# Optimization experiments

Measured on AMD Instinct MI355X. Metric: run time of the kernel, lower is better.

The kernel has to match this reference:

```python
import jax, jax.numpy as jnp
import numpy as np

N_NODES = 50000
N_EDGES = 800000
IN_C = 16
HID_C = 16
OUT_C = 10
N_GRAPHS = 500
EDGE_DIM = 3
MLP_HID = 25
BN_EPS = 1e-5


def setup_inputs() -> dict:
    key = jax.random.key(0)
    ks = iter(jax.random.split(key, 40))

    def nrm(shape, scale=1.0):
        return jax.random.normal(next(ks), shape, dtype=jnp.float32) * scale

    inp = {}
    inp["x"] = nrm((N_NODES, IN_C))
    inp["edge_index"] = jax.random.randint(next(ks), (2, N_EDGES), 0, N_NODES, dtype=jnp.int32)
    inp["edge_attr"] = jax.random.uniform(next(ks), (N_EDGES, EDGE_DIM), dtype=jnp.float32)
    inp["batch"] = jnp.sort(jax.random.randint(next(ks), (N_NODES,), 0, N_GRAPHS, dtype=jnp.int32))

    def bn_params():
        g = jax.random.uniform(next(ks), (MLP_HID,), minval=0.8, maxval=1.2, dtype=jnp.float32)
        b = nrm((MLP_HID,), 0.1)
        mu = nrm((MLP_HID,), 0.1)
        var = jax.random.uniform(next(ks), (MLP_HID,), minval=0.5, maxval=1.5, dtype=jnp.float32)
        return g, b, mu, var

    # edge MLP 1: 3 -> 25 -> IN_C*HID_C
    inp["W1a"] = nrm((EDGE_DIM, MLP_HID), 0.3)
    inp["b1a"] = nrm((MLP_HID,), 0.05)
    inp["g1"], inp["bt1"], inp["m1"], inp["v1"] = bn_params()
    inp["W1b"] = nrm((MLP_HID, IN_C * HID_C), 0.1)
    inp["b1b"] = nrm((IN_C * HID_C,), 0.05)
    inp["root1"] = nrm((IN_C, HID_C), 0.2)
    inp["bias1"] = nrm((HID_C,), 0.05)

    # edge MLP 2: 3 -> 25 -> HID_C*HID_C
    inp["W2a"] = nrm((EDGE_DIM, MLP_HID), 0.3)
    inp["b2a"] = nrm((MLP_HID,), 0.05)
    inp["g2"], inp["bt2"], inp["m2"], inp["v2"] = bn_params()
    inp["W2b"] = nrm((MLP_HID, HID_C * HID_C), 0.1)
    inp["b2b"] = nrm((HID_C * HID_C,), 0.05)
    inp["root2"] = nrm((HID_C, HID_C), 0.2)
    inp["bias2"] = nrm((HID_C,), 0.05)

    # final MLP([HID_C, OUT_C]) -> single plain linear (plain_last)
    inp["fcW"] = nrm((HID_C, OUT_C), 0.2)
    inp["fcb"] = nrm((OUT_C,), 0.05)
    return inp


def _edge_mlp(e, Wa, ba, g, bt, mu, var, Wb, bb):
    # Linear -> BatchNorm(eval) -> ReLU -> (dropout=eval identity) -> Linear
    h = e @ Wa + ba
    h = g * (h - mu) * jax.lax.rsqrt(var + BN_EPS) + bt
    h = jax.nn.relu(h)
    return h @ Wb + bb


def _nnconv(x, src, dst, w_edge, root, bias, out_dim):
    # message: x_j [E,in] times per-edge weight [E,in,out]
    msg = jnp.einsum("ei,eio->eo", x[src], w_edge)
    agg = jax.ops.segment_sum(msg, dst, num_segments=N_NODES)
    deg = jax.ops.segment_sum(jnp.ones((src.shape[0],), msg.dtype), dst, num_segments=N_NODES)
    agg = agg / jnp.maximum(deg, 1.0)[:, None]  # mean aggregation
    return agg + x @ root + bias


def reference(x, edge_index, edge_attr, batch,
              W1a, b1a, g1, bt1, m1, v1, W1b, b1b, root1, bias1,
              W2a, b2a, g2, bt2, m2, v2, W2b, b2b, root2, bias2,
              fcW, fcb):
    src, dst = edge_index[0], edge_index[1]

    w1 = _edge_mlp(edge_attr, W1a, b1a, g1, bt1, m1, v1, W1b, b1b).reshape(-1, IN_C, HID_C)
    x = jax.nn.elu(_nnconv(x, src, dst, w1, root1, bias1, HID_C))

    w2 = _edge_mlp(edge_attr, W2a, b2a, g2, bt2, m2, v2, W2b, b2b).reshape(-1, HID_C, HID_C)
    x = jax.nn.elu(_nnconv(x, src, dst, w2, root2, bias2, HID_C))

    # global mean pooling over graphs
    pooled = jax.ops.segment_sum(x, batch, num_segments=N_GRAPHS)
    cnt = jax.ops.segment_sum(jnp.ones((x.shape[0],), x.dtype), batch, num_segments=N_GRAPHS)
    pooled = pooled / jnp.maximum(cnt, 1.0)[:, None]

    return pooled @ fcW + fcb  # [N_GRAPHS, OUT_C]
```

## Files before the change

### kernel.cpp

```cpp
#include <hip/hip_runtime.h>
#include <math.h>

#define N_NODES 50000
#define N_EDGES 800000
#define IN_C 16
#define HID_C 16
#define OUT_C 10
#define N_GRAPHS 500
#define EDGE_DIM 3
#define MLP_HID 25
#define BN_EPS 1e-5f

#define SCAN_NB ((N_NODES + 255) / 256)

typedef __attribute__((ext_vector_type(8))) short short8;
typedef __attribute__((ext_vector_type(4))) float f32x4;
union U4S8 { uint4 u; short8 s; };


__global__ __launch_bounds__(256) void prep_graph_kernel(
    const float* __restrict__ W1a, const float* __restrict__ b1a,
    const float* __restrict__ g1, const float* __restrict__ bt1,
    const float* __restrict__ m1, const float* __restrict__ v1,
    const float* __restrict__ W2a, const float* __restrict__ b2a,
    const float* __restrict__ g2, const float* __restrict__ bt2,
    const float* __restrict__ m2, const float* __restrict__ v2,
    const int* __restrict__ batch,
    float* __restrict__ AC1, float* __restrict__ AC2,
    int* __restrict__ goff)
{
    int t = threadIdx.x;
    if (blockIdx.x == 0) {
        if (t < 26) {
            int k = t;
            if (k < 25) {
                float sc = g1[k] / sqrtf(v1[k] + BN_EPS);
                AC1[k*4+0] = sc * W1a[0*MLP_HID+k];
                AC1[k*4+1] = sc * W1a[1*MLP_HID+k];
                AC1[k*4+2] = sc * W1a[2*MLP_HID+k];
                AC1[k*4+3] = sc * (b1a[k] - m1[k]) + bt1[k];
            } else {
                AC1[100] = 0.f; AC1[101] = 0.f; AC1[102] = 0.f; AC1[103] = 1.f;
            }
        } else if (t >= 32 && t < 58) {
            int k = t - 32;
            if (k < 25) {
                float sc = g2[k] / sqrtf(v2[k] + BN_EPS);
                AC2[k*4+0] = sc * W2a[0*MLP_HID+k];
                AC2[k*4+1] = sc * W2a[1*MLP_HID+k];
                AC2[k*4+2] = sc * W2a[2*MLP_HID+k];
                AC2[k*4+3] = sc * (b2a[k] - m2[k]) + bt2[k];
            } else {
                AC2[100] = 0.f; AC2[101] = 0.f; AC2[102] = 0.f; AC2[103] = 1.f;
            }
        }
    }
    int g = blockIdx.x * blockDim.x + t;
    if (g <= N_GRAPHS) {
        int lo = 0, hi = N_NODES;
        while (lo < hi) {
            int mid = (lo + hi) >> 1;
            if (batch[mid] < g) lo = mid + 1; else hi = mid;
        }
        goff[g] = lo;
    }
}

__global__ __launch_bounds__(256) void pack_w_kernel(
    const float* __restrict__ W1b, const float* __restrict__ b1b,
    const float* __restrict__ W2b, const float* __restrict__ b2b,
    unsigned int* __restrict__ WHI1, unsigned int* __restrict__ WLO1,
    unsigned int* __restrict__ WHI2, unsigned int* __restrict__ WLO2)
{
    int t = blockIdx.x * 256 + threadIdx.x;
    if (t >= 1664) return;
    const float *Wb, *bb; unsigned int *WH, *WL;
    int tl = t;
    if (t < 832) { Wb = W1b; bb = b1b; WH = WHI1; WL = WLO1; }
    else { tl = t - 832; Wb = W2b; bb = b2b; WH = WHI2; WL = WLO2; }
    int m = tl >> 6;
    int L = tl & 63;
    int q = L >> 4, o = L & 15;
    unsigned int hi[8], lo[8];
    for (int j = 0; j < 8; ++j) {
        int kp = m*32 + q*8 + j;
        int k = kp >> 4, i = kp & 15;
        float w = (k < 25) ? Wb[k*256 + i*16 + o] : bb[i*16 + o];
        unsigned int u = __float_as_uint(w);
        unsigned int h = (u + 0x7FFFu + ((u >> 16) & 1u)) >> 16;
        hi[j] = h;
        float rl = w - __uint_as_float(h << 16);
        unsigned int ul = __float_as_uint(rl);
        lo[j] = (ul + 0x7FFFu + ((ul >> 16) & 1u)) >> 16;
    }
    int base = (m*64 + L) * 4;
    for (int d = 0; d < 4; ++d) {
        WH[base + d] = hi[2*d] | (hi[2*d+1] << 16);
        WL[base + d] = lo[2*d] | (lo[2*d+1] << 16);
    }
}


__global__ __launch_bounds__(256) void rank_kernel(const int* __restrict__ dst,
                                                   int* __restrict__ cnt,
                                                   int* __restrict__ rank) {
    int e = blockIdx.x * blockDim.x + threadIdx.x;
    if (e < N_EDGES) rank[e] = atomicAdd(&cnt[dst[e]], 1);
}

__global__ __launch_bounds__(256) void scan_p1(const int* __restrict__ cnt,
                                               int* __restrict__ bsum) {
    __shared__ int lds[256];
    int t = threadIdx.x;
    int idx = blockIdx.x * 256 + t;
    lds[t] = (idx < N_NODES) ? cnt[idx] : 0;
    __syncthreads();
    for (int d = 128; d > 0; d >>= 1) {
        if (t < d) lds[t] += lds[t + d];
        __syncthreads();
    }
    if (t == 0) bsum[blockIdx.x] = lds[0];
}

__global__ __launch_bounds__(256) void scan_p2(const int* __restrict__ bsum,
                                               int* __restrict__ bpre,
                                               int* __restrict__ off) {
    __shared__ int lds[256];
    int t = threadIdx.x;
    lds[t] = (t < SCAN_NB) ? bsum[t] : 0;
    __syncthreads();
    for (int d = 1; d < 256; d <<= 1) {
        int v = (t >= d) ? lds[t - d] : 0;
        __syncthreads();
        lds[t] += v;
        __syncthreads();
    }
    if (t < SCAN_NB) bpre[t] = (t > 0) ? lds[t - 1] : 0;
    if (t == 255) off[N_NODES] = lds[255];
}

__global__ __launch_bounds__(256) void scan_p3(const int* __restrict__ cnt,
                                               const int* __restrict__ bpre,
                                               int* __restrict__ off) {
    __shared__ int lds[256];
    int t = threadIdx.x;
    int idx = blockIdx.x * 256 + t;
    int v = (idx < N_NODES) ? cnt[idx] : 0;
    lds[t] = v;
    __syncthreads();
    for (int d = 1; d < 256; d <<= 1) {
        int u = (t >= d) ? lds[t - d] : 0;
        __syncthreads();
        lds[t] += u;
        __syncthreads();
    }
    if (idx < N_NODES) off[idx] = bpre[blockIdx.x] + lds[t] - v;
}


__global__ __launch_bounds__(256) void edge_mfma_kernel(
    const float* __restrict__ xin,
    const int* __restrict__ src, const int* __restrict__ dst,
    const int* __restrict__ rank, const int* __restrict__ off,
    const float* __restrict__ eattr,
    const float* __restrict__ AC,
    const unsigned int* __restrict__ WHI, const unsigned int* __restrict__ WLO,
    float* __restrict__ msg_buf)
{
    __shared__ uint4 wlo_s[832];
    __shared__ float ac_s[104];
    __shared__ __attribute__((aligned(16))) float xs_s[4][16][16];
    __shared__ __attribute__((aligned(16))) float ea_s[4][16][4];
    __shared__ int   pp_s[4][16];

    const int tid = threadIdx.x;
    #pragma unroll
    for (int it = 0; it < 4; ++it) {
        int gi = tid + it*256;
        if (gi < 832) wlo_s[gi] = ((const uint4*)WLO)[gi];
    }
    if (tid < 104) ac_s[tid] = AC[tid];
    __syncthreads();

    const int wave = tid >> 6;
    const int lane = tid & 63;
    const int q = lane >> 4;

    short8 whi[13];
    #pragma unroll
    for (int m = 0; m < 13; ++m) {
        U4S8 c; c.u = ((const uint4*)WHI)[m*64 + lane];
        whi[m] = c.s;
    }

    const int tile = blockIdx.x * 4 + wave;
    const int e0 = tile * 16;

    {
        int el = lane >> 2, part = lane & 3;
        int s = src[e0 + el];
        const float4 v = ((const float4*)(xin + (size_t)s * IN_C))[part];
        *(float4*)&xs_s[wave][el][part*4] = v;
    }
    if (lane < 48) {
        int c = lane >> 4, e = lane & 15;
        ea_s[wave][e][c] = eattr[(size_t)(e0 + e)*3 + c];
    }
    if (lane < 16) {
        int e = e0 + lane;
        pp_s[wave][lane] = off[dst[e]] + rank[e];
    }

    const int e = lane & 15;
    const int i0 = (q & 1) * 8;
    const float4 ea = *(const float4*)&ea_s[wave][e][0];
    const float a0 = ea.x, a1 = ea.y, a2 = ea.z;
    float x8[8];
    {
        float4 v0 = *(const float4*)&xs_s[wave][e][i0];
        float4 v1 = *(const float4*)&xs_s[wave][e][i0 + 4];
        x8[0]=v0.x; x8[1]=v0.y; x8[2]=v0.z; x8[3]=v0.w;
        x8[4]=v1.x; x8[5]=v1.y; x8[6]=v1.z; x8[7]=v1.w;
    }

    f32x4 acc = {0.f, 0.f, 0.f, 0.f};
    #pragma unroll
    for (int m = 0; m < 13; ++m) {
        int k = 2*m + (q >> 1);
        const float4 A = *(const float4*)&ac_s[k*4];
        float hk = fmaxf(fmaf(a2, A.z, fmaf(a1, A.y, fmaf(a0, A.x, A.w))), 0.f);
        unsigned int pd0, pd1, pd2, pd3;
        {
            unsigned int b0 = __float_as_uint(hk * x8[0]);
            unsigned int b1 = __float_as_uint(hk * x8[1]);
            pd0 = __builtin_amdgcn_perm(b1, b0, 0x07060302u);
            unsigned int b2 = __float_as_uint(hk * x8[2]);
            unsigned int b3 = __float_as_uint(hk * x8[3]);
            pd1 = __builtin_amdgcn_perm(b3, b2, 0x07060302u);
            unsigned int b4 = __float_as_uint(hk * x8[4]);
            unsigned int b5 = __float_as_uint(hk * x8[5]);
            pd2 = __builtin_amdgcn_perm(b5, b4, 0x07060302u);
            unsigned int b6 = __float_as_uint(hk * x8[6]);
            unsigned int b7 = __float_as_uint(hk * x8[7]);
            pd3 = __builtin_amdgcn_perm(b7, b6, 0x07060302u);
        }
        U4S8 af; af.u = make_uint4(pd0, pd1, pd2, pd3);
        U4S8 wl; wl.u = wlo_s[m*64 + lane];
        acc = __builtin_amdgcn_mfma_f32_16x16x32_bf16(af.s, whi[m], acc, 0, 0, 0);
        acc = __builtin_amdgcn_mfma_f32_16x16x32_bf16(af.s, wl.s,   acc, 0, 0, 0);
    }

    const int o = lane & 15;
    #pragma unroll
    for (int r = 0; r < 4; ++r) {
        int p = pp_s[wave][q*4 + r];
        msg_buf[(size_t)p * HID_C + o] = acc[r];
    }
}

__global__ __launch_bounds__(256) void node_gather_kernel(
    const float* __restrict__ xin, const float* __restrict__ msg_buf,
    const int* __restrict__ off,
    const float* __restrict__ root, const float* __restrict__ bias,
    float* __restrict__ xout)
{
    int t = blockIdx.x * blockDim.x + threadIdx.x;
    int n = t >> 4;
    int o = t & 15;
    if (n >= N_NODES) return;
    int lo = off[n], hi = off[n+1];
    float inv = 1.f / fmaxf((float)(hi - lo), 1.f);

    float s0 = 0.f, s1 = 0.f, s2 = 0.f, s3 = 0.f;
    int r = lo;
    for (; r + 4 <= hi; r += 4) {
        s0 += msg_buf[(size_t)r     * HID_C + o];
        s1 += msg_buf[(size_t)(r+1) * HID_C + o];
        s2 += msg_buf[(size_t)(r+2) * HID_C + o];
        s3 += msg_buf[(size_t)(r+3) * HID_C + o];
    }
    for (; r < hi; ++r) s0 += msg_buf[(size_t)r * HID_C + o];
    float s = (s0 + s1) + (s2 + s3);

    float acc = fmaf(s, inv, bias[o]);
    const float* xr = xin + (size_t)n * IN_C;
    #pragma unroll
    for (int i = 0; i < IN_C; ++i)
        acc = fmaf(xr[i], root[i*HID_C+o], acc);
    xout[(size_t)n*HID_C + o] = acc > 0.f ? acc : (expf(acc) - 1.f);
}

__global__ __launch_bounds__(64) void pool_final_kernel(
    const float* __restrict__ xin, const int* __restrict__ goff,
    const float* __restrict__ fcW, const float* __restrict__ fcb,
    float* __restrict__ out)
{
    __shared__ float part[4][HID_C];
    __shared__ float pooled[HID_C];
    int g = blockIdx.x;
    int t = threadIdx.x;
    int c = t & 15, sub = t >> 4;
    int lo = goff[g], hi = goff[g+1];
    float s = 0.f;
    for (int n = lo + sub; n < hi; n += 4)
        s += xin[(size_t)n*HID_C + c];
    part[sub][c] = s;
    __syncthreads();
    if (t < HID_C) {
        pooled[t] = (part[0][t] + part[1][t] + part[2][t] + part[3][t])
                    / fmaxf((float)(hi - lo), 1.f);
    }
    __syncthreads();
    if (t < OUT_C) {
        float acc = fcb[t];
        #pragma unroll
        for (int i = 0; i < HID_C; ++i)
            acc = fmaf(pooled[i], fcW[i*OUT_C+t], acc);
        out[g*OUT_C + t] = acc;
    }
}


extern "C" void kernel_launch(void* const* d_in, const int* in_sizes, int n_in,
                              void* d_out, int out_size, void* d_ws, size_t ws_size,
                              hipStream_t stream)
{
    const float* x     = (const float*)d_in[0];
    const int*   ei    = (const int*)d_in[1];
    const float* eattr = (const float*)d_in[2];
    const int*   batch = (const int*)d_in[3];
    const float* W1a   = (const float*)d_in[4];
    const float* b1a   = (const float*)d_in[5];
    const float* g1    = (const float*)d_in[6];
    const float* bt1   = (const float*)d_in[7];
    const float* m1    = (const float*)d_in[8];
    const float* v1    = (const float*)d_in[9];
    const float* W1b   = (const float*)d_in[10];
    const float* b1b   = (const float*)d_in[11];
    const float* root1 = (const float*)d_in[12];
    const float* bias1 = (const float*)d_in[13];
    const float* W2a   = (const float*)d_in[14];
    const float* b2a   = (const float*)d_in[15];
    const float* g2    = (const float*)d_in[16];
    const float* bt2   = (const float*)d_in[17];
    const float* m2    = (const float*)d_in[18];
    const float* v2    = (const float*)d_in[19];
    const float* W2b   = (const float*)d_in[20];
    const float* b2b   = (const float*)d_in[21];
    const float* root2 = (const float*)d_in[22];
    const float* bias2 = (const float*)d_in[23];
    const float* fcW   = (const float*)d_in[24];
    const float* fcb   = (const float*)d_in[25];

    const int* src = ei;
    const int* dst = ei + N_EDGES;

    float* ws   = (float*)d_ws;
    float* MSG  = ws;
    float* X1   = ws + 12800000;
    float* X2   = ws + 13600000;
    int*   RANK = (int*)(ws + 14400000);
    int*   CNT  = (int*)(ws + 15200000);
    int*   OFF  = (int*)(ws + 15250000);
    int*   GOFF = (int*)(ws + 15300064);
    unsigned int* WHI1 = (unsigned int*)(ws + 15300576);
    unsigned int* WLO1 = (unsigned int*)(ws + 15303904);
    unsigned int* WHI2 = (unsigned int*)(ws + 15307232);
    unsigned int* WLO2 = (unsigned int*)(ws + 15310560);
    float* AC1  = ws + 15313888;
    float* AC2  = ws + 15314000;
    int*   BSUM = (int*)(ws + 15314112);
    int*   BPRE = (int*)(ws + 15314368);

    hipMemsetAsync(CNT, 0, N_NODES * sizeof(int), stream);
    prep_graph_kernel<<<3, 256, 0, stream>>>(W1a, b1a, g1, bt1, m1, v1,
                                             W2a, b2a, g2, bt2, m2, v2,
                                             batch, AC1, AC2, GOFF);
    pack_w_kernel<<<7, 256, 0, stream>>>(W1b, b1b, W2b, b2b,
                                         WHI1, WLO1, WHI2, WLO2);
    rank_kernel<<<N_EDGES/256, 256, 0, stream>>>(dst, CNT, RANK);
    scan_p1<<<SCAN_NB, 256, 0, stream>>>(CNT, BSUM);
    scan_p2<<<1, 256, 0, stream>>>(BSUM, BPRE, OFF);
    scan_p3<<<SCAN_NB, 256, 0, stream>>>(CNT, BPRE, OFF);

    edge_mfma_kernel<<<N_EDGES/64, 256, 0, stream>>>(x, src, dst, RANK, OFF,
                                                     eattr, AC1, WHI1, WLO1, MSG);
    node_gather_kernel<<<(N_NODES*16+255)/256, 256, 0, stream>>>(x, MSG, OFF,
                                                                 root1, bias1, X1);

    edge_mfma_kernel<<<N_EDGES/64, 256, 0, stream>>>(X1, src, dst, RANK, OFF,
                                                     eattr, AC2, WHI2, WLO2, MSG);
    node_gather_kernel<<<(N_NODES*16+255)/256, 256, 0, stream>>>(X1, MSG, OFF,
                                                                 root2, bias2, X2);

    pool_final_kernel<<<N_GRAPHS, 64, 0, stream>>>(X2, GOFF, fcW, fcb, (float*)d_out);
}
```

Before: 309.9 us.

## Precompute edge scatter positions and process four edge tiles per wave

A new small kernel computes each edge's final scatter position (off[dst]+rank) once and stores it, so both edge passes read it directly instead of recomputing it through a dependent gather. The edge kernel now has each wave handle 64 edges in four 16-edge tiles. Per-edge attributes, sources and positions are loaded into registers up front, and the next tile's x row is prefetched while the current tile runs its MFMAs. LDS staging and the per-tile shared-memory round trip are removed. This amortizes the per-block weight loads to LDS and registers over four times as many edges, at the cost of higher register pressure and 4x fewer blocks.

```diff
diff --git a/kernel.cpp b/kernel.cpp
--- a/kernel.cpp
+++ b/kernel.cpp
@@ -15,6 +15,7 @@
 
 typedef __attribute__((ext_vector_type(8))) short short8;
 typedef __attribute__((ext_vector_type(4))) float f32x4;
+typedef __attribute__((ext_vector_type(2))) float f32x2;
 union U4S8 { uint4 u; short8 s; };
 
 
@@ -157,11 +158,32 @@
     if (idx < N_NODES) off[idx] = bpre[blockIdx.x] + lds[t] - v;
 }
 
-
-__global__ __launch_bounds__(256) void edge_mfma_kernel(
+__global__ __launch_bounds__(256) void pos2_kernel(const int* __restrict__ dst,
+                                                   const int* __restrict__ off,
+                                                   int* __restrict__ rank) {
+    int e = blockIdx.x * blockDim.x + threadIdx.x;
+    if (e < N_EDGES) rank[e] = off[dst[e]] + rank[e];
+}
+
+
+__device__ __forceinline__ U4S8 packH(float h, float4 xl, float4 xh) {
+    f32x2 h2; h2.x = h; h2.y = h;
+    f32x2 m0; m0.x = xl.x; m0.y = xl.y; m0 *= h2;
+    f32x2 m1; m1.x = xl.z; m1.y = xl.w; m1 *= h2;
+    f32x2 m2; m2.x = xh.x; m2.y = xh.y; m2 *= h2;
+    f32x2 m3; m3.x = xh.z; m3.y = xh.w; m3 *= h2;
+    U4S8 r;
+    r.u.x = __builtin_amdgcn_perm(__float_as_uint(m0.y), __float_as_uint(m0.x), 0x07060302u);
+    r.u.y = __builtin_amdgcn_perm(__float_as_uint(m1.y), __float_as_uint(m1.x), 0x07060302u);
+    r.u.z = __builtin_amdgcn_perm(__float_as_uint(m2.y), __float_as_uint(m2.x), 0x07060302u);
+    r.u.w = __builtin_amdgcn_perm(__float_as_uint(m3.y), __float_as_uint(m3.x), 0x07060302u);
+    return r;
+}
+
+__global__ __launch_bounds__(256) void edge_mfma2_kernel(
     const float* __restrict__ xin,
-    const int* __restrict__ src, const int* __restrict__ dst,
-    const int* __restrict__ rank, const int* __restrict__ off,
+    const int* __restrict__ src,
+    const int* __restrict__ P,
     const float* __restrict__ eattr,
     const float* __restrict__ AC,
     const unsigned int* __restrict__ WHI, const unsigned int* __restrict__ WLO,
@@ -169,10 +191,6 @@
 {
     __shared__ uint4 wlo_s[832];
     __shared__ float ac_s[104];
-    __shared__ __attribute__((aligned(16))) float xs_s[4][16][16];
-    __shared__ __attribute__((aligned(16))) float ea_s[4][16][4];
-    __shared__ int   pp_s[4][16];
-
     const int tid = threadIdx.x;
     #pragma unroll
     for (int it = 0; it < 4; ++it) {
@@ -184,7 +202,9 @@
 
     const int wave = tid >> 6;
     const int lane = tid & 63;
-    const int q = lane >> 4;
+    const int q    = lane >> 4;
+    const int el   = lane & 15;
+    const int i0   = (q & 1) * 8;
 
     short8 whi[13];
     #pragma unroll
@@ -193,68 +213,52 @@
         whi[m] = c.s;
     }
 
-    const int tile = blockIdx.x * 4 + wave;
-    const int e0 = tile * 16;
-
+    const int We = blockIdx.x * 256 + wave * 64;
+
+    int   ss[4]; float ax[4], ay[4], az[4]; uint4 pp[4];
+    #pragma unroll
+    for (int t = 0; t < 4; ++t) {
+        int e = We + t*16 + el;
+        ss[t] = src[e];
+        ax[t] = eattr[(size_t)e*3+0];
+        ay[t] = eattr[(size_t)e*3+1];
+        az[t] = eattr[(size_t)e*3+2];
+        pp[t] = *(const uint4*)(P + We + t*16 + q*4);
+    }
+
+    float4 xl, xh;
     {
-        int el = lane >> 2, part = lane & 3;
-        int s = src[e0 + el];
-        const float4 v = ((const float4*)(xin + (size_t)s * IN_C))[part];
-        *(float4*)&xs_s[wave][el][part*4] = v;
-    }
-    if (lane < 48) {
-        int c = lane >> 4, e = lane & 15;
-        ea_s[wave][e][c] = eattr[(size_t)(e0 + e)*3 + c];
-    }
-    if (lane < 16) {
-        int e = e0 + lane;
-        pp_s[wave][lane] = off[dst[e]] + rank[e];
-    }
-
-    const int e = lane & 15;
-    const int i0 = (q & 1) * 8;
-    const float4 ea = *(const float4*)&ea_s[wave][e][0];
-    const float a0 = ea.x, a1 = ea.y, a2 = ea.z;
-    float x8[8];
-    {
-        float4 v0 = *(const float4*)&xs_s[wave][e][i0];
-        float4 v1 = *(const float4*)&xs_s[wave][e][i0 + 4];
-        x8[0]=v0.x; x8[1]=v0.y; x8[2]=v0.z; x8[3]=v0.w;
-        x8[4]=v1.x; x8[5]=v1.y; x8[6]=v1.z; x8[7]=v1.w;
-    }
-
-    f32x4 acc = {0.f, 0.f, 0.f, 0.f};
+        const float4* xp = (const float4*)(xin + (size_t)ss[0]*16 + i0);
+        xl = xp[0]; xh = xp[1];
+    }
+
     #pragma unroll
-    for (int m = 0; m < 13; ++m) {
-        int k = 2*m + (q >> 1);
-        const float4 A = *(const float4*)&ac_s[k*4];
-        float hk = fmaxf(fmaf(a2, A.z, fmaf(a1, A.y, fmaf(a0, A.x, A.w))), 0.f);
-        unsigned int pd0, pd1, pd2, pd3;
-        {
-            unsigned int b0 = __float_as_uint(hk * x8[0]);
-            unsigned int b1 = __float_as_uint(hk * x8[1]);
-            pd0 = __builtin_amdgcn_perm(b1, b0, 0x07060302u);
-            unsigned int b2 = __float_as_uint(hk * x8[2]);
-            unsigned int b3 = __float_as_uint(hk * x8[3]);
-            pd1 = __builtin_amdgcn_perm(b3, b2, 0x07060302u);
-            unsigned int b4 = __float_as_uint(hk * x8[4]);
-            unsigned int b5 = __float_as_uint(hk * x8[5]);
-            pd2 = __builtin_amdgcn_perm(b5, b4, 0x07060302u);
-            unsigned int b6 = __float_as_uint(hk * x8[6]);
-            unsigned int b7 = __float_as_uint(hk * x8[7]);
-            pd3 = __builtin_amdgcn_perm(b7, b6, 0x07060302u);
+    for (int t = 0; t < 4; ++t) {
+        float4 nxl, nxh;
+        if (t < 3) {
+            const float4* xp = (const float4*)(xin + (size_t)ss[t+1]*16 + i0);
+            nxl = xp[0]; nxh = xp[1];
         }
-        U4S8 af; af.u = make_uint4(pd0, pd1, pd2, pd3);
-        U4S8 wl; wl.u = wlo_s[m*64 + lane];
-        acc = __builtin_amdgcn_mfma_f32_16x16x32_bf16(af.s, whi[m], acc, 0, 0, 0);
-        acc = __builtin_amdgcn_mfma_f32_16x16x32_bf16(af.s, wl.s,   acc, 0, 0, 0);
-    }
-
-    const int o = lane & 15;
-    #pragma unroll
-    for (int r = 0; r < 4; ++r) {
-        int p = pp_s[wave][q*4 + r];
-        msg_buf[(size_t)p * HID_C + o] = acc[r];
+
+        f32x4 acc = {0.f, 0.f, 0.f, 0.f};
+        #pragma unroll
+        for (int m = 0; m < 13; ++m) {
+            int k = 2*m + (q >> 1);
+            const float4 Ak = *(const float4*)&ac_s[k*4];
+            U4S8 wl; wl.u = wlo_s[m*64 + lane];
+            float h = fmaxf(fmaf(az[t], Ak.z, fmaf(ay[t], Ak.y,
+                              fmaf(ax[t], Ak.x, Ak.w))), 0.f);
+            U4S8 hf = packH(h, xl, xh);
+            acc = __builtin_amdgcn_mfma_f32_16x16x32_bf16(hf.s, whi[m], acc, 0, 0, 0);
+            acc = __builtin_amdgcn_mfma_f32_16x16x32_bf16(hf.s, wl.s,   acc, 0, 0, 0);
+        }
+
+        msg_buf[(size_t)((unsigned)pp[t].x) * HID_C + el] = acc[0];
+        msg_buf[(size_t)((unsigned)pp[t].y) * HID_C + el] = acc[1];
+        msg_buf[(size_t)((unsigned)pp[t].z) * HID_C + el] = acc[2];
+        msg_buf[(size_t)((unsigned)pp[t].w) * HID_C + el] = acc[3];
+
+        xl = nxl; xh = nxh;
     }
 }
 
@@ -382,14 +386,15 @@
     scan_p1<<<SCAN_NB, 256, 0, stream>>>(CNT, BSUM);
     scan_p2<<<1, 256, 0, stream>>>(BSUM, BPRE, OFF);
     scan_p3<<<SCAN_NB, 256, 0, stream>>>(CNT, BPRE, OFF);
-
-    edge_mfma_kernel<<<N_EDGES/64, 256, 0, stream>>>(x, src, dst, RANK, OFF,
-                                                     eattr, AC1, WHI1, WLO1, MSG);
+    pos2_kernel<<<N_EDGES/256, 256, 0, stream>>>(dst, OFF, RANK);
+
+    edge_mfma2_kernel<<<N_EDGES/256, 256, 0, stream>>>(x, src, RANK, eattr,
+                                                       AC1, WHI1, WLO1, MSG);
     node_gather_kernel<<<(N_NODES*16+255)/256, 256, 0, stream>>>(x, MSG, OFF,
                                                                  root1, bias1, X1);
 
-    edge_mfma_kernel<<<N_EDGES/64, 256, 0, stream>>>(X1, src, dst, RANK, OFF,
-                                                     eattr, AC2, WHI2, WLO2, MSG);
+    edge_mfma2_kernel<<<N_EDGES/256, 256, 0, stream>>>(X1, src, RANK, eattr,
+                                                       AC2, WHI2, WLO2, MSG);
     node_gather_kernel<<<(N_NODES*16+255)/256, 256, 0, stream>>>(X1, MSG, OFF,
                                                                  root2, bias2, X2);
 
```

Result: slower. 364.4 us (+17.6%).
